# Performance work log

Hardware: AMD Instinct MI355X
Metric: run time of the kernel (lower is better)

## Reference

```python
import jax, jax.numpy as jnp
import numpy as np

HIDDEN = 32
FEATURES = 16
LABELS = 4
T = 8
N = 40000
E = 640000
D_IN = FEATURES + LABELS + HIDDEN + 1  # GATv2Conv input dim = 53


def setup_inputs() -> dict:
    key = jax.random.key(0)
    ks = jax.random.split(key, 16)
    x = jax.random.normal(ks[0], (T, N, FEATURES), dtype=jnp.float32)
    mask = (jax.random.uniform(ks[1], (N,)) < 0.7).astype(jnp.float32)
    labels = jax.random.normal(ks[2], (N, LABELS), dtype=jnp.float32)
    edge_index = jax.random.randint(ks[3], (2, E), 0, N, dtype=jnp.int32)
    edge_weight = jax.random.uniform(ks[4], (E,), dtype=jnp.float32)
    s = 1.0 / np.sqrt(D_IN)
    # 4 GATv2Conv layers stacked: 0=reset, 1=update, 2=cell, 3=final
    Wl = jax.random.normal(ks[5], (4, HIDDEN, D_IN), dtype=jnp.float32) * s
    bl = jnp.zeros((4, HIDDEN), dtype=jnp.float32)
    Wr = jax.random.normal(ks[6], (4, HIDDEN, D_IN), dtype=jnp.float32) * s
    br = jnp.zeros((4, HIDDEN), dtype=jnp.float32)
    att = jax.random.normal(ks[7], (4, HIDDEN), dtype=jnp.float32) * (1.0 / np.sqrt(HIDDEN))
    bconv = jnp.zeros((4, HIDDEN), dtype=jnp.float32)
    W1 = jax.random.normal(ks[8], (FEATURES, HIDDEN), dtype=jnp.float32) * (1.0 / np.sqrt(HIDDEN))
    b1 = jnp.zeros((FEATURES,), dtype=jnp.float32)
    W2 = jax.random.normal(ks[9], (FEATURES, 2 * HIDDEN), dtype=jnp.float32) * (1.0 / np.sqrt(2 * HIDDEN))
    b2 = jnp.zeros((FEATURES,), dtype=jnp.float32)
    return {"x": x, "mask": mask, "labels": labels, "edge_index": edge_index,
            "edge_weight": edge_weight, "Wl": Wl, "bl": bl, "Wr": Wr, "br": br,
            "att": att, "bconv": bconv, "W1": W1, "b1": b1, "W2": W2, "b2": b2}


def gatv2(xin, src, dst, Wl, bl, Wr, br, att, bconv):
    # GATv2Conv, heads=1, add_self_loops=False (edge_weight unused: lin_edge is None)
    xl = xin @ Wl.T + bl          # [N, H] source transform (message)
    xr = xin @ Wr.T + br          # [N, H] target transform
    z = jax.nn.leaky_relu(xl[src] + xr[dst], 0.2)  # [E, H]
    e = z @ att                   # [E] attention logits
    m = jax.ops.segment_max(e, dst, num_segments=N)
    a = jnp.exp(e - m[dst])
    den = jax.ops.segment_sum(a, dst, num_segments=N)[dst]
    a = a / jnp.where(den > 0, den, 1.0)
    out = jax.ops.segment_sum(a[:, None] * xl[src], dst, num_segments=N)
    return out + bconv


def reference(x, mask, labels, edge_index, edge_weight, Wl, bl, Wr, br, att, bconv, W1, b1, W2, b2):
    src, dst = edge_index[0], edge_index[1]
    mcol = mask[:, None]                       # [N, 1] float, concatenated as a feature
    mbool = mcol > 0.5                         # [N, 1] bool, used for where()
    masked_input = jnp.where(mbool[None], x, 0.0)  # [T, N, F]
    hidden0 = jnp.ones((N, HIDDEN), dtype=x.dtype)
    x2_0 = masked_input[0]

    def step(carry, xt):
        hidden, x2 = carry
        ft = jnp.concatenate([x2, mcol, labels], axis=1)        # [N, F+1+L]
        inp = jnp.concatenate([ft, hidden], axis=1)             # [N, D_IN]
        reset = jax.nn.sigmoid(gatv2(inp, src, dst, Wl[0], bl[0], Wr[0], br[0], att[0], bconv[0]))
        update = jax.nn.sigmoid(gatv2(inp, src, dst, Wl[1], bl[1], Wr[1], br[1], att[1], bconv[1]))
        cin = jnp.concatenate([ft, reset * hidden], axis=1)
        cell = jnp.tanh(gatv2(cin, src, dst, Wl[2], bl[2], Wr[2], br[2], att[2], bconv[2]))
        hidden = update * hidden + (1.0 - update) * cell        # (dropout inactive: eval mode)
        y1 = hidden @ W1.T + b1
        x1 = jnp.where(mbool, xt, y1)
        ft2 = jnp.concatenate([x1, mcol, hidden, labels], axis=1)  # [N, D_IN]
        s = jax.nn.relu(gatv2(ft2, src, dst, Wl[3], bl[3], Wr[3], br[3], att[3], bconv[3]))
        y2 = jnp.concatenate([s, hidden], axis=1) @ W2.T + b2
        x2_new = jnp.where(mbool, xt, y2)
        return (hidden, x2_new), x2_new

    _, out = jax.lax.scan(step, (hidden0, x2_0), masked_input)
    return out  # [T, N, F]
```

## Files before the change

### kernel.cpp

```cpp
#include <hip/hip_runtime.h>
#include <math.h>

#define NN   40000
#define EE   640000
#define HID  32
#define FEAT 16
#define LAB  4
#define TT   8
#define DIN  53


__global__ __launch_bounds__(256) void zero_i32(int* __restrict__ p, int n) {
    int i = blockIdx.x * 256 + threadIdx.x;
    if (i < n) p[i] = 0;
}

__global__ __launch_bounds__(256) void hist_kernel(const int* __restrict__ dst,
                                                   int* __restrict__ deg) {
    int e = blockIdx.x * 256 + threadIdx.x;
    if (e < EE) atomicAdd(&deg[dst[e]], 1);
}

__global__ __launch_bounds__(1024) void scan_kernel(const int* __restrict__ deg,
                                                    int* __restrict__ row_ptr) {
    __shared__ int wsum[16];
    __shared__ int chunk_total;
    int tid = threadIdx.x;
    int lane = tid & 63, wv = tid >> 6;
    int carry = 0;
    if (tid == 0) row_ptr[0] = 0;
    for (int base = 0; base < NN; base += 1024) {
        int i = base + tid;
        int v = (i < NN) ? deg[i] : 0;
        #pragma unroll
        for (int o = 1; o < 64; o <<= 1) {
            int t = __shfl_up(v, o);
            if (lane >= o) v += t;
        }
        if (lane == 63) wsum[wv] = v;
        __syncthreads();
        if (tid < 16) {
            int s = wsum[tid];
            #pragma unroll
            for (int o = 1; o < 16; o <<= 1) {
                int t = __shfl_up(s, o);
                if (tid >= o) s += t;
            }
            wsum[tid] = s;
            if (tid == 15) chunk_total = s;
        }
        __syncthreads();
        int woff = (wv == 0) ? 0 : wsum[wv - 1];
        if (i < NN) row_ptr[i + 1] = carry + woff + v;
        carry += chunk_total;
        __syncthreads();
    }
}

__global__ __launch_bounds__(256) void scatter_kernel(const int* __restrict__ src,
                                                      const int* __restrict__ dst,
                                                      const int* __restrict__ row_ptr,
                                                      int* __restrict__ cursor,
                                                      int* __restrict__ csr_src) {
    int e = blockIdx.x * 256 + threadIdx.x;
    if (e < EE) {
        int d = dst[e];
        int pos = atomicAdd(&cursor[d], 1);
        csr_src[row_ptr[d] + pos] = src[e];
    }
}


__global__ __launch_bounds__(256) void init_kernel(const float* __restrict__ x0,
                                                   const float* __restrict__ mask,
                                                   float* __restrict__ hidden,
                                                   float* __restrict__ x2) {
    int i = blockIdx.x * 256 + threadIdx.x;
    if (i < NN * HID) hidden[i] = 1.0f;
    if (i < NN * FEAT) {
        int node = i >> 4;
        x2[i] = (mask[node] > 0.5f) ? x0[i] : 0.0f;
    }
}


template <bool HMUL>
__global__ __launch_bounds__(256) void dense_kernel(const float* __restrict__ feat,
                                                    const float* __restrict__ mask,
                                                    const float* __restrict__ labels,
                                                    const float* __restrict__ hsrc,
                                                    const float* __restrict__ hmul,
                                                    const float* __restrict__ Wl,
                                                    const float* __restrict__ bl,
                                                    const float* __restrict__ Wr,
                                                    const float* __restrict__ br,
                                                    float* __restrict__ xl,
                                                    float* __restrict__ xr) {
    __shared__ float Wl_s[HID * DIN];
    __shared__ float Wr_s[HID * DIN];
    __shared__ float inp_s[8][DIN];
    for (int idx = threadIdx.x; idx < HID * DIN; idx += 256) {
        Wl_s[idx] = Wl[idx];
        Wr_s[idx] = Wr[idx];
    }
    int ni = threadIdx.x >> 5, k = threadIdx.x & 31;
    int node = blockIdx.x * 8 + ni;
    for (int i = k; i < DIN; i += 32) {
        float v;
        if (i < 16)       v = feat[node * 16 + i];
        else if (i == 16) v = mask[node];
        else if (i < 21)  v = labels[node * 4 + (i - 17)];
        else {
            v = hsrc[node * 32 + (i - 21)];
            if (HMUL) v *= hmul[node * 32 + (i - 21)];
        }
        inp_s[ni][i] = v;
    }
    __syncthreads();
    float al = bl[k], ar = br[k];
    const float* wlr = &Wl_s[k * DIN];
    const float* wrr = &Wr_s[k * DIN];
#pragma unroll
    for (int i = 0; i < DIN; ++i) {
        float xv = inp_s[ni][i];
        al += xv * wlr[i];
        ar += xv * wrr[i];
    }
    xl[node * 32 + k] = al;
    xr[node * 32 + k] = ar;
}

template <int ACT>
__global__ __launch_bounds__(256) void conv_kernel(const int* __restrict__ row_ptr,
                                                   const int* __restrict__ csr_src,
                                                   const float* __restrict__ xl,
                                                   const float* __restrict__ xr,
                                                   const float* __restrict__ att,
                                                   const float* __restrict__ bconv,
                                                   float* __restrict__ out) {
    int wid  = threadIdx.x >> 6;
    int lane = threadIdx.x & 63;
    int g = lane >> 2;
    int j = lane & 3;
    int n = blockIdx.x * 4 + wid;
    int c0 = j * 8;
    int beg = row_ptr[n], end = row_ptr[n + 1];

    float4 at0 = *(const float4*)(att + c0);
    float4 at1 = *(const float4*)(att + c0 + 4);
    float4 xr0 = *(const float4*)(xr + n * 32 + c0);
    float4 xr1 = *(const float4*)(xr + n * 32 + c0 + 4);

    float m = -INFINITY, den = 0.0f;
    float acc[8] = {0, 0, 0, 0, 0, 0, 0, 0};

    for (int p = beg + g; p < end; p += 16) {
        int s = csr_src[p];
        const float4* rp = (const float4*)(xl + s * 32 + c0);
        float4 v0 = rp[0];
        float4 v1 = rp[1];
        float part, z;
        z = v0.x + xr0.x; z = (z > 0.f) ? z : 0.2f * z; part  = z * at0.x;
        z = v0.y + xr0.y; z = (z > 0.f) ? z : 0.2f * z; part += z * at0.y;
        z = v0.z + xr0.z; z = (z > 0.f) ? z : 0.2f * z; part += z * at0.z;
        z = v0.w + xr0.w; z = (z > 0.f) ? z : 0.2f * z; part += z * at0.w;
        z = v1.x + xr1.x; z = (z > 0.f) ? z : 0.2f * z; part += z * at1.x;
        z = v1.y + xr1.y; z = (z > 0.f) ? z : 0.2f * z; part += z * at1.y;
        z = v1.z + xr1.z; z = (z > 0.f) ? z : 0.2f * z; part += z * at1.z;
        z = v1.w + xr1.w; z = (z > 0.f) ? z : 0.2f * z; part += z * at1.w;
        part += __shfl_xor(part, 1);
        part += __shfl_xor(part, 2);
        float e = part;
        if (e > m) {
            float sc = __expf(m - e);
            den *= sc;
#pragma unroll
            for (int i = 0; i < 8; ++i) acc[i] *= sc;
            m = e;
        }
        float a = __expf(e - m);
        den += a;
        acc[0] += a * v0.x; acc[1] += a * v0.y; acc[2] += a * v0.z; acc[3] += a * v0.w;
        acc[4] += a * v1.x; acc[5] += a * v1.y; acc[6] += a * v1.z; acc[7] += a * v1.w;
    }

    float o[8];
    if (beg < end) {
        float mt = m;
        mt = fmaxf(mt, __shfl_xor(mt, 4));
        mt = fmaxf(mt, __shfl_xor(mt, 8));
        mt = fmaxf(mt, __shfl_xor(mt, 16));
        mt = fmaxf(mt, __shfl_xor(mt, 32));
        float sc = __expf(m - mt);
        float d = den * sc;
        d += __shfl_xor(d, 4);
        d += __shfl_xor(d, 8);
        d += __shfl_xor(d, 16);
        d += __shfl_xor(d, 32);
#pragma unroll
        for (int i = 0; i < 8; ++i) {
            float t = acc[i] * sc;
            t += __shfl_xor(t, 4);
            t += __shfl_xor(t, 8);
            t += __shfl_xor(t, 16);
            t += __shfl_xor(t, 32);
            o[i] = t / d;
        }
    } else {
#pragma unroll
        for (int i = 0; i < 8; ++i) o[i] = 0.0f;
    }

    if (g == 0) {
        float4 bc0 = *(const float4*)(bconv + c0);
        float4 bc1 = *(const float4*)(bconv + c0 + 4);
        float r[8];
        r[0] = o[0] + bc0.x; r[1] = o[1] + bc0.y; r[2] = o[2] + bc0.z; r[3] = o[3] + bc0.w;
        r[4] = o[4] + bc1.x; r[5] = o[5] + bc1.y; r[6] = o[6] + bc1.z; r[7] = o[7] + bc1.w;
#pragma unroll
        for (int i = 0; i < 8; ++i) {
            if (ACT == 0)      r[i] = 1.0f / (1.0f + __expf(-r[i]));
            else if (ACT == 1) r[i] = tanhf(r[i]);
            else               r[i] = fmaxf(r[i], 0.0f);
        }
        float4* op = (float4*)(out + n * 32 + c0);
        op[0] = make_float4(r[0], r[1], r[2], r[3]);
        op[1] = make_float4(r[4], r[5], r[6], r[7]);
    }
}


__global__ __launch_bounds__(256) void update_dense3_kernel(
        const float* __restrict__ g_update, const float* __restrict__ g_cell,
        float* __restrict__ hidden,
        const float* __restrict__ x_t, const float* __restrict__ mask,
        const float* __restrict__ labels,
        const float* __restrict__ W1, const float* __restrict__ b1,
        const float* __restrict__ Wl3, const float* __restrict__ bl3,
        const float* __restrict__ Wr3, const float* __restrict__ br3,
        float* __restrict__ xl, float* __restrict__ xr) {
    __shared__ float Wl_s[HID * DIN];
    __shared__ float Wr_s[HID * DIN];
    __shared__ float W1_s[FEAT * HID];
    __shared__ float inp_s[8][DIN];
    __shared__ float hs[8][HID + 1];
    for (int idx = threadIdx.x; idx < HID * DIN; idx += 256) {
        Wl_s[idx] = Wl3[idx];
        Wr_s[idx] = Wr3[idx];
    }
    for (int idx = threadIdx.x; idx < FEAT * HID; idx += 256) W1_s[idx] = W1[idx];
    int ni = threadIdx.x >> 5, k = threadIdx.x & 31;
    int node = blockIdx.x * 8 + ni;
    float u = g_update[node * 32 + k];
    float c = g_cell[node * 32 + k];
    float h = hidden[node * 32 + k];
    float hn = u * h + (1.0f - u) * c;
    hidden[node * 32 + k] = hn;
    hs[ni][k] = hn;
    inp_s[ni][17 + k] = hn;
    if (k == 0) inp_s[ni][16] = mask[node];
    if (k < 4)  inp_s[ni][49 + k] = labels[node * 4 + k];
    __syncthreads();
    if (k < 16) {
        float a = b1[k];
        const float* w = &W1_s[k * 32];
#pragma unroll
        for (int i = 0; i < 32; ++i) a += hs[ni][i] * w[i];
        float mv = mask[node];
        inp_s[ni][k] = (mv > 0.5f) ? x_t[node * 16 + k] : a;
    }
    __syncthreads();
    float al = bl3[k], ar = br3[k];
    const float* wl = &Wl_s[k * DIN];
    const float* wr = &Wr_s[k * DIN];
#pragma unroll
    for (int i = 0; i < DIN; ++i) {
        float xv = inp_s[ni][i];
        al += xv * wl[i];
        ar += xv * wr[i];
    }
    xl[node * 32 + k] = al;
    xr[node * 32 + k] = ar;
}


__global__ __launch_bounds__(256) void out_kernel(const float* __restrict__ s,
                                                  const float* __restrict__ hidden,
                                                  const float* __restrict__ W2,
                                                  const float* __restrict__ b2,
                                                  const float* __restrict__ x_t,
                                                  const float* __restrict__ mask,
                                                  float* __restrict__ x2,
                                                  float* __restrict__ out_t) {
    int ni = threadIdx.x >> 4, f = threadIdx.x & 15;
    int node = blockIdx.x * 16 + ni;
    float acc = b2[f];
    const float* srow = s + node * 32;
    const float* hrow = hidden + node * 32;
    const float* w = W2 + f * 64;
#pragma unroll
    for (int i = 0; i < 32; ++i) acc += srow[i] * w[i];
#pragma unroll
    for (int i = 0; i < 32; ++i) acc += hrow[i] * w[32 + i];
    float mv = mask[node];
    float xv = x_t[node * 16 + f];
    float r = (mv > 0.5f) ? xv : acc;
    x2[node * 16 + f] = r;
    out_t[node * 16 + f] = r;
}


extern "C" void kernel_launch(void* const* d_in, const int* in_sizes, int n_in,
                              void* d_out, int out_size, void* d_ws, size_t ws_size,
                              hipStream_t stream) {
    const float* x      = (const float*)d_in[0];
    const float* mask   = (const float*)d_in[1];
    const float* labels = (const float*)d_in[2];
    const int*   src    = (const int*)d_in[3];
    const int*   dst    = src + EE;
    const float* Wl    = (const float*)d_in[5];
    const float* bl    = (const float*)d_in[6];
    const float* Wr    = (const float*)d_in[7];
    const float* br    = (const float*)d_in[8];
    const float* att   = (const float*)d_in[9];
    const float* bconv = (const float*)d_in[10];
    const float* W1    = (const float*)d_in[11];
    const float* b1    = (const float*)d_in[12];
    const float* W2    = (const float*)d_in[13];
    const float* b2    = (const float*)d_in[14];
    float* out = (float*)d_out;

    char* ws = (char*)d_ws;
    size_t off = 0;
    auto alloc = [&](size_t bytes) -> void* {
        void* p = ws + off;
        off = (off + bytes + 255) & ~(size_t)255;
        return p;
    };
    int*   row_ptr = (int*)alloc((NN + 1) * sizeof(int));
    int*   deg     = (int*)alloc(NN * sizeof(int));
    int*   csr_src = (int*)alloc(EE * sizeof(int));
    float* hidden  = (float*)alloc(NN * HID * sizeof(float));
    float* x2      = (float*)alloc(NN * FEAT * sizeof(float));
    float* xl      = (float*)alloc(NN * HID * sizeof(float));
    float* xr      = (float*)alloc(NN * HID * sizeof(float));
    float* g0      = (float*)alloc(NN * HID * sizeof(float));
    float* g1      = (float*)alloc(NN * HID * sizeof(float));
    float* g2      = (float*)alloc(NN * HID * sizeof(float));

    const int WD = HID * DIN;

    zero_i32<<<(NN + 255) / 256, 256, 0, stream>>>(deg, NN);
    hist_kernel<<<EE / 256, 256, 0, stream>>>(dst, deg);
    scan_kernel<<<1, 1024, 0, stream>>>(deg, row_ptr);
    zero_i32<<<(NN + 255) / 256, 256, 0, stream>>>(deg, NN);
    scatter_kernel<<<EE / 256, 256, 0, stream>>>(src, dst, row_ptr, deg, csr_src);
    init_kernel<<<NN * HID / 256, 256, 0, stream>>>(x, mask, hidden, x2);

    for (int t = 0; t < TT; ++t) {
        const float* xt = x + (size_t)t * NN * FEAT;
        float* out_t = out + (size_t)t * NN * FEAT;
        dense_kernel<false><<<NN / 8, 256, 0, stream>>>(x2, mask, labels, hidden, nullptr,
            Wl + 0 * WD, bl + 0 * HID, Wr + 0 * WD, br + 0 * HID, xl, xr);
        conv_kernel<0><<<NN / 4, 256, 0, stream>>>(row_ptr, csr_src, xl, xr,
            att + 0 * HID, bconv + 0 * HID, g0);
        dense_kernel<false><<<NN / 8, 256, 0, stream>>>(x2, mask, labels, hidden, nullptr,
            Wl + 1 * WD, bl + 1 * HID, Wr + 1 * WD, br + 1 * HID, xl, xr);
        conv_kernel<0><<<NN / 4, 256, 0, stream>>>(row_ptr, csr_src, xl, xr,
            att + 1 * HID, bconv + 1 * HID, g1);
        dense_kernel<true><<<NN / 8, 256, 0, stream>>>(x2, mask, labels, hidden, g0,
            Wl + 2 * WD, bl + 2 * HID, Wr + 2 * WD, br + 2 * HID, xl, xr);
        conv_kernel<1><<<NN / 4, 256, 0, stream>>>(row_ptr, csr_src, xl, xr,
            att + 2 * HID, bconv + 2 * HID, g2);
        update_dense3_kernel<<<NN / 8, 256, 0, stream>>>(g1, g2, hidden, xt, mask, labels,
            W1, b1, Wl + 3 * WD, bl + 3 * HID, Wr + 3 * WD, br + 3 * HID, xl, xr);
        conv_kernel<2><<<NN / 4, 256, 0, stream>>>(row_ptr, csr_src, xl, xr,
            att + 3 * HID, bconv + 3 * HID, g0);
        out_kernel<<<NN / 16, 256, 0, stream>>>(g0, hidden, W2, b2, xt, mask, x2, out_t);
    }
}
```

Baseline: 1.999 ms.

## Fuse reset/update GATv2 layers and fold output projection into final conv

The reset and update gates share the same input, so their dense transforms and edge-aggregation passes are merged into one kernel each. The two layers' features are stored interleaved as 64-wide rows, so a single CSR traversal gathers both. The final conv kernel now also computes the W2 output projection and mask select in-register via shuffles, which removes out_kernel and the round trip of the s buffer through memory. The trade-offs are more registers and LDS per block in the merged kernels, possibly lower occupancy, and a W2 transpose load on every conv3 block.

```diff
diff --git a/kernel.cpp b/kernel.cpp
--- a/kernel.cpp
+++ b/kernel.cpp
@@ -8,6 +8,7 @@
 #define LAB  4
 #define TT   8
 #define DIN  53
+#define WD   (HID * DIN)
 
 
 __global__ __launch_bounds__(256) void zero_i32(int* __restrict__ p, int n) {
@@ -84,7 +85,55 @@
 }
 
 
-template <bool HMUL>
+__global__ __launch_bounds__(256) void dense01_kernel(const float* __restrict__ feat,
+                                                      const float* __restrict__ mask,
+                                                      const float* __restrict__ labels,
+                                                      const float* __restrict__ hsrc,
+                                                      const float* __restrict__ Wl,
+                                                      const float* __restrict__ bl,
+                                                      const float* __restrict__ Wr,
+                                                      const float* __restrict__ br,
+                                                      float* __restrict__ xl01,
+                                                      float* __restrict__ xr01) {
+    __shared__ float W_s[4 * WD];
+    __shared__ float inp_s[8][DIN];
+    for (int idx = threadIdx.x; idx < WD; idx += 256) {
+        W_s[idx]          = Wl[idx];
+        W_s[WD + idx]     = Wl[WD + idx];
+        W_s[2 * WD + idx] = Wr[idx];
+        W_s[3 * WD + idx] = Wr[WD + idx];
+    }
+    int ni = threadIdx.x >> 5, k = threadIdx.x & 31;
+    int node = blockIdx.x * 8 + ni;
+    for (int i = k; i < DIN; i += 32) {
+        float v;
+        if (i < 16)       v = feat[node * 16 + i];
+        else if (i == 16) v = mask[node];
+        else if (i < 21)  v = labels[node * 4 + (i - 17)];
+        else              v = hsrc[node * 32 + (i - 21)];
+        inp_s[ni][i] = v;
+    }
+    __syncthreads();
+    float l0 = bl[k], l1 = bl[HID + k], r0 = br[k], r1 = br[HID + k];
+    const float* w0 = &W_s[k * DIN];
+    const float* w1 = &W_s[WD + k * DIN];
+    const float* w2 = &W_s[2 * WD + k * DIN];
+    const float* w3 = &W_s[3 * WD + k * DIN];
+#pragma unroll
+    for (int i = 0; i < DIN; ++i) {
+        float xv = inp_s[ni][i];
+        l0 += xv * w0[i];
+        l1 += xv * w1[i];
+        r0 += xv * w2[i];
+        r1 += xv * w3[i];
+    }
+    xl01[node * 64 + k]      = l0;
+    xl01[node * 64 + 32 + k] = l1;
+    xr01[node * 64 + k]      = r0;
+    xr01[node * 64 + 32 + k] = r1;
+}
+
+
 __global__ __launch_bounds__(256) void dense_kernel(const float* __restrict__ feat,
                                                     const float* __restrict__ mask,
                                                     const float* __restrict__ labels,
@@ -96,10 +145,10 @@
                                                     const float* __restrict__ br,
                                                     float* __restrict__ xl,
                                                     float* __restrict__ xr) {
-    __shared__ float Wl_s[HID * DIN];
-    __shared__ float Wr_s[HID * DIN];
+    __shared__ float Wl_s[WD];
+    __shared__ float Wr_s[WD];
     __shared__ float inp_s[8][DIN];
-    for (int idx = threadIdx.x; idx < HID * DIN; idx += 256) {
+    for (int idx = threadIdx.x; idx < WD; idx += 256) {
         Wl_s[idx] = Wl[idx];
         Wr_s[idx] = Wr[idx];
     }
@@ -110,10 +159,7 @@
         if (i < 16)       v = feat[node * 16 + i];
         else if (i == 16) v = mask[node];
         else if (i < 21)  v = labels[node * 4 + (i - 17)];
-        else {
-            v = hsrc[node * 32 + (i - 21)];
-            if (HMUL) v *= hmul[node * 32 + (i - 21)];
-        }
+        else              v = hsrc[node * 32 + (i - 21)] * hmul[node * 32 + (i - 21)];
         inp_s[ni][i] = v;
     }
     __syncthreads();
@@ -130,62 +176,42 @@
     xr[node * 32 + k] = ar;
 }
 
-template <int ACT>
-__global__ __launch_bounds__(256) void conv_kernel(const int* __restrict__ row_ptr,
-                                                   const int* __restrict__ csr_src,
-                                                   const float* __restrict__ xl,
-                                                   const float* __restrict__ xr,
-                                                   const float* __restrict__ att,
-                                                   const float* __restrict__ bconv,
-                                                   float* __restrict__ out) {
-    int wid  = threadIdx.x >> 6;
-    int lane = threadIdx.x & 63;
-    int g = lane >> 2;
-    int j = lane & 3;
-    int n = blockIdx.x * 4 + wid;
-    int c0 = j * 8;
-    int beg = row_ptr[n], end = row_ptr[n + 1];
-
-    float4 at0 = *(const float4*)(att + c0);
-    float4 at1 = *(const float4*)(att + c0 + 4);
-    float4 xr0 = *(const float4*)(xr + n * 32 + c0);
-    float4 xr1 = *(const float4*)(xr + n * 32 + c0 + 4);
-
-    float m = -INFINITY, den = 0.0f;
-    float acc[8] = {0, 0, 0, 0, 0, 0, 0, 0};
-
-    for (int p = beg + g; p < end; p += 16) {
-        int s = csr_src[p];
-        const float4* rp = (const float4*)(xl + s * 32 + c0);
-        float4 v0 = rp[0];
-        float4 v1 = rp[1];
-        float part, z;
-        z = v0.x + xr0.x; z = (z > 0.f) ? z : 0.2f * z; part  = z * at0.x;
-        z = v0.y + xr0.y; z = (z > 0.f) ? z : 0.2f * z; part += z * at0.y;
-        z = v0.z + xr0.z; z = (z > 0.f) ? z : 0.2f * z; part += z * at0.z;
-        z = v0.w + xr0.w; z = (z > 0.f) ? z : 0.2f * z; part += z * at0.w;
-        z = v1.x + xr1.x; z = (z > 0.f) ? z : 0.2f * z; part += z * at1.x;
-        z = v1.y + xr1.y; z = (z > 0.f) ? z : 0.2f * z; part += z * at1.y;
-        z = v1.z + xr1.z; z = (z > 0.f) ? z : 0.2f * z; part += z * at1.z;
-        z = v1.w + xr1.w; z = (z > 0.f) ? z : 0.2f * z; part += z * at1.w;
-        part += __shfl_xor(part, 1);
-        part += __shfl_xor(part, 2);
-        float e = part;
-        if (e > m) {
-            float sc = __expf(m - e);
-            den *= sc;
-#pragma unroll
-            for (int i = 0; i < 8; ++i) acc[i] *= sc;
-            m = e;
-        }
-        float a = __expf(e - m);
-        den += a;
-        acc[0] += a * v0.x; acc[1] += a * v0.y; acc[2] += a * v0.z; acc[3] += a * v0.w;
-        acc[4] += a * v1.x; acc[5] += a * v1.y; acc[6] += a * v1.z; acc[7] += a * v1.w;
-    }
-
-    float o[8];
-    if (beg < end) {
+
+__device__ __forceinline__ float edge_score(const float4& v0, const float4& v1,
+                                            const float4& xr0, const float4& xr1,
+                                            const float4& at0, const float4& at1) {
+    float part, z;
+    z = v0.x + xr0.x; z = (z > 0.f) ? z : 0.2f * z; part  = z * at0.x;
+    z = v0.y + xr0.y; z = (z > 0.f) ? z : 0.2f * z; part += z * at0.y;
+    z = v0.z + xr0.z; z = (z > 0.f) ? z : 0.2f * z; part += z * at0.z;
+    z = v0.w + xr0.w; z = (z > 0.f) ? z : 0.2f * z; part += z * at0.w;
+    z = v1.x + xr1.x; z = (z > 0.f) ? z : 0.2f * z; part += z * at1.x;
+    z = v1.y + xr1.y; z = (z > 0.f) ? z : 0.2f * z; part += z * at1.y;
+    z = v1.z + xr1.z; z = (z > 0.f) ? z : 0.2f * z; part += z * at1.z;
+    z = v1.w + xr1.w; z = (z > 0.f) ? z : 0.2f * z; part += z * at1.w;
+    part += __shfl_xor(part, 1);
+    part += __shfl_xor(part, 2);
+    return part;
+}
+
+__device__ __forceinline__ void online_update(float e, float& m, float& den, float* acc,
+                                              const float4& v0, const float4& v1) {
+    if (e > m) {
+        float sc = __expf(m - e);
+        den *= sc;
+#pragma unroll
+        for (int i = 0; i < 8; ++i) acc[i] *= sc;
+        m = e;
+    }
+    float a = __expf(e - m);
+    den += a;
+    acc[0] += a * v0.x; acc[1] += a * v0.y; acc[2] += a * v0.z; acc[3] += a * v0.w;
+    acc[4] += a * v1.x; acc[5] += a * v1.y; acc[6] += a * v1.z; acc[7] += a * v1.w;
+}
+
+__device__ __forceinline__ void merge_groups(float m, float den, const float* acc,
+                                             bool nonempty, float* o) {
+    if (nonempty) {
         float mt = m;
         mt = fmaxf(mt, __shfl_xor(mt, 4));
         mt = fmaxf(mt, __shfl_xor(mt, 8));
@@ -210,22 +236,194 @@
 #pragma unroll
         for (int i = 0; i < 8; ++i) o[i] = 0.0f;
     }
+}
+
+
+__global__ __launch_bounds__(256) void conv01_kernel(const int* __restrict__ row_ptr,
+                                                     const int* __restrict__ csr_src,
+                                                     const float* __restrict__ xl01,
+                                                     const float* __restrict__ xr01,
+                                                     const float* __restrict__ att,
+                                                     const float* __restrict__ bconv,
+                                                     float* __restrict__ g0,
+                                                     float* __restrict__ g1) {
+    int wid  = threadIdx.x >> 6;
+    int lane = threadIdx.x & 63;
+    int g = lane >> 2, j = lane & 3;
+    int n = blockIdx.x * 4 + wid;
+    int c0 = j * 8;
+    int beg = row_ptr[n], end = row_ptr[n + 1];
+
+    float4 a00 = *(const float4*)(att + c0);
+    float4 a01 = *(const float4*)(att + c0 + 4);
+    float4 a10 = *(const float4*)(att + 32 + c0);
+    float4 a11 = *(const float4*)(att + 32 + c0 + 4);
+    const float* xrn = xr01 + n * 64;
+    float4 xr00 = *(const float4*)(xrn + c0);
+    float4 xr01v = *(const float4*)(xrn + c0 + 4);
+    float4 xr10 = *(const float4*)(xrn + 32 + c0);
+    float4 xr11 = *(const float4*)(xrn + 32 + c0 + 4);
+
+    float m0 = -INFINITY, den0 = 0.0f, acc0[8] = {0, 0, 0, 0, 0, 0, 0, 0};
+    float m1 = -INFINITY, den1 = 0.0f, acc1[8] = {0, 0, 0, 0, 0, 0, 0, 0};
+
+    for (int p = beg + g; p < end; p += 16) {
+        int s = csr_src[p];
+        const float4* rp = (const float4*)(xl01 + s * 64 + c0);
+        const float4* rq = (const float4*)(xl01 + s * 64 + 32 + c0);
+        float4 v00 = rp[0], v01 = rp[1];
+        float4 v10 = rq[0], v11 = rq[1];
+        float e0 = edge_score(v00, v01, xr00, xr01v, a00, a01);
+        float e1 = edge_score(v10, v11, xr10, xr11, a10, a11);
+        online_update(e0, m0, den0, acc0, v00, v01);
+        online_update(e1, m1, den1, acc1, v10, v11);
+    }
+
+    float o0[8], o1[8];
+    bool ne = beg < end;
+    merge_groups(m0, den0, acc0, ne, o0);
+    merge_groups(m1, den1, acc1, ne, o1);
+
+    if (g == 0) {
+        float4 b00 = *(const float4*)(bconv + c0);
+        float4 b01 = *(const float4*)(bconv + c0 + 4);
+        float4 b10 = *(const float4*)(bconv + 32 + c0);
+        float4 b11 = *(const float4*)(bconv + 32 + c0 + 4);
+        float r0[8] = {o0[0] + b00.x, o0[1] + b00.y, o0[2] + b00.z, o0[3] + b00.w,
+                       o0[4] + b01.x, o0[5] + b01.y, o0[6] + b01.z, o0[7] + b01.w};
+        float r1[8] = {o1[0] + b10.x, o1[1] + b10.y, o1[2] + b10.z, o1[3] + b10.w,
+                       o1[4] + b11.x, o1[5] + b11.y, o1[6] + b11.z, o1[7] + b11.w};
+#pragma unroll
+        for (int i = 0; i < 8; ++i) {
+            r0[i] = 1.0f / (1.0f + __expf(-r0[i]));
+            r1[i] = 1.0f / (1.0f + __expf(-r1[i]));
+        }
+        float4* p0 = (float4*)(g0 + n * 32 + c0);
+        p0[0] = make_float4(r0[0], r0[1], r0[2], r0[3]);
+        p0[1] = make_float4(r0[4], r0[5], r0[6], r0[7]);
+        float4* p1 = (float4*)(g1 + n * 32 + c0);
+        p1[0] = make_float4(r1[0], r1[1], r1[2], r1[3]);
+        p1[1] = make_float4(r1[4], r1[5], r1[6], r1[7]);
+    }
+}
+
+
+__global__ __launch_bounds__(256) void conv2_kernel(const int* __restrict__ row_ptr,
+                                                    const int* __restrict__ csr_src,
+                                                    const float* __restrict__ xl,
+                                                    const float* __restrict__ xr,
+                                                    const float* __restrict__ att,
+                                                    const float* __restrict__ bconv,
+                                                    float* __restrict__ out) {
+    int wid  = threadIdx.x >> 6;
+    int lane = threadIdx.x & 63;
+    int g = lane >> 2, j = lane & 3;
+    int n = blockIdx.x * 4 + wid;
+    int c0 = j * 8;
+    int beg = row_ptr[n], end = row_ptr[n + 1];
+
+    float4 at0 = *(const float4*)(att + c0);
+    float4 at1 = *(const float4*)(att + c0 + 4);
+    float4 xr0 = *(const float4*)(xr + n * 32 + c0);
+    float4 xr1 = *(const float4*)(xr + n * 32 + c0 + 4);
+
+    float m = -INFINITY, den = 0.0f, acc[8] = {0, 0, 0, 0, 0, 0, 0, 0};
+    for (int p = beg + g; p < end; p += 16) {
+        int s = csr_src[p];
+        const float4* rp = (const float4*)(xl + s * 32 + c0);
+        float4 v0 = rp[0], v1 = rp[1];
+        float e = edge_score(v0, v1, xr0, xr1, at0, at1);
+        online_update(e, m, den, acc, v0, v1);
+    }
+    float o[8];
+    merge_groups(m, den, acc, beg < end, o);
 
     if (g == 0) {
         float4 bc0 = *(const float4*)(bconv + c0);
         float4 bc1 = *(const float4*)(bconv + c0 + 4);
-        float r[8];
-        r[0] = o[0] + bc0.x; r[1] = o[1] + bc0.y; r[2] = o[2] + bc0.z; r[3] = o[3] + bc0.w;
-        r[4] = o[4] + bc1.x; r[5] = o[5] + bc1.y; r[6] = o[6] + bc1.z; r[7] = o[7] + bc1.w;
-#pragma unroll
-        for (int i = 0; i < 8; ++i) {
-            if (ACT == 0)      r[i] = 1.0f / (1.0f + __expf(-r[i]));
-            else if (ACT == 1) r[i] = tanhf(r[i]);
-            else               r[i] = fmaxf(r[i], 0.0f);
-        }
+        float r[8] = {o[0] + bc0.x, o[1] + bc0.y, o[2] + bc0.z, o[3] + bc0.w,
+                      o[4] + bc1.x, o[5] + bc1.y, o[6] + bc1.z, o[7] + bc1.w};
+#pragma unroll
+        for (int i = 0; i < 8; ++i) r[i] = tanhf(r[i]);
         float4* op = (float4*)(out + n * 32 + c0);
         op[0] = make_float4(r[0], r[1], r[2], r[3]);
         op[1] = make_float4(r[4], r[5], r[6], r[7]);
+    }
+}
+
+
+__global__ __launch_bounds__(256) void conv3_out_kernel(const int* __restrict__ row_ptr,
+                                                        const int* __restrict__ csr_src,
+                                                        const float* __restrict__ xl,
+                                                        const float* __restrict__ xr,
+                                                        const float* __restrict__ att,
+                                                        const float* __restrict__ bconv,
+                                                        const float* __restrict__ hidden,
+                                                        const float* __restrict__ W2,
+                                                        const float* __restrict__ b2,
+                                                        const float* __restrict__ x_t,
+                                                        const float* __restrict__ mask,
+                                                        float* __restrict__ x2,
+                                                        float* __restrict__ out_t) {
+    __shared__ float W2s[64 * 16];
+    for (int idx = threadIdx.x; idx < 64 * 16; idx += 256) {
+        int f = idx & 15, c = idx >> 4;
+        W2s[c * 16 + f] = W2[f * 64 + c];
+    }
+    __syncthreads();
+
+    int wid  = threadIdx.x >> 6;
+    int lane = threadIdx.x & 63;
+    int g = lane >> 2, j = lane & 3;
+    int n = blockIdx.x * 4 + wid;
+    int c0 = j * 8;
+    int beg = row_ptr[n], end = row_ptr[n + 1];
+
+    float4 at0 = *(const float4*)(att + c0);
+    float4 at1 = *(const float4*)(att + c0 + 4);
+    float4 xr0 = *(const float4*)(xr + n * 32 + c0);
+    float4 xr1 = *(const float4*)(xr + n * 32 + c0 + 4);
+
+    float m = -INFINITY, den = 0.0f, acc[8] = {0, 0, 0, 0, 0, 0, 0, 0};
+    for (int p = beg + g; p < end; p += 16) {
+        int s = csr_src[p];
+        const float4* rp = (const float4*)(xl + s * 32 + c0);
+        float4 v0 = rp[0], v1 = rp[1];
+        float e = edge_score(v0, v1, xr0, xr1, at0, at1);
+        online_update(e, m, den, acc, v0, v1);
+    }
+    float o[8];
+    merge_groups(m, den, acc, beg < end, o);
+
+    float4 bc0 = *(const float4*)(bconv + c0);
+    float4 bc1 = *(const float4*)(bconv + c0 + 4);
+    float r[8] = {fmaxf(o[0] + bc0.x, 0.f), fmaxf(o[1] + bc0.y, 0.f),
+                  fmaxf(o[2] + bc0.z, 0.f), fmaxf(o[3] + bc0.w, 0.f),
+                  fmaxf(o[4] + bc1.x, 0.f), fmaxf(o[5] + bc1.y, 0.f),
+                  fmaxf(o[6] + bc1.z, 0.f), fmaxf(o[7] + bc1.w, 0.f)};
+    float4 h0 = *(const float4*)(hidden + n * 32 + c0);
+    float4 h1 = *(const float4*)(hidden + n * 32 + c0 + 4);
+    float hv[8] = {h0.x, h0.y, h0.z, h0.w, h1.x, h1.y, h1.z, h1.w};
+
+    int f = lane & 15;
+    int base = lane & ~3;
+    float y = b2[f];
+#pragma unroll
+    for (int j2 = 0; j2 < 4; ++j2) {
+#pragma unroll
+        for (int i = 0; i < 8; ++i) {
+            float sv = __shfl(r[i], base + j2);
+            float hh = __shfl(hv[i], base + j2);
+            int c = j2 * 8 + i;
+            y += sv * W2s[c * 16 + f] + hh * W2s[(32 + c) * 16 + f];
+        }
+    }
+    if (lane < 16) {
+        float mv = mask[n];
+        float xv = x_t[n * 16 + f];
+        float rr = (mv > 0.5f) ? xv : y;
+        x2[n * 16 + f] = rr;
+        out_t[n * 16 + f] = rr;
     }
 }
 
@@ -239,12 +437,12 @@
         const float* __restrict__ Wl3, const float* __restrict__ bl3,
         const float* __restrict__ Wr3, const float* __restrict__ br3,
         float* __restrict__ xl, float* __restrict__ xr) {
-    __shared__ float Wl_s[HID * DIN];
-    __shared__ float Wr_s[HID * DIN];
+    __shared__ float Wl_s[WD];
+    __shared__ float Wr_s[WD];
     __shared__ float W1_s[FEAT * HID];
     __shared__ float inp_s[8][DIN];
     __shared__ float hs[8][HID + 1];
-    for (int idx = threadIdx.x; idx < HID * DIN; idx += 256) {
+    for (int idx = threadIdx.x; idx < WD; idx += 256) {
         Wl_s[idx] = Wl3[idx];
         Wr_s[idx] = Wr3[idx];
     }
@@ -281,32 +479,6 @@
     }
     xl[node * 32 + k] = al;
     xr[node * 32 + k] = ar;
-}
-
-
-__global__ __launch_bounds__(256) void out_kernel(const float* __restrict__ s,
-                                                  const float* __restrict__ hidden,
-                                                  const float* __restrict__ W2,
-                                                  const float* __restrict__ b2,
-                                                  const float* __restrict__ x_t,
-                                                  const float* __restrict__ mask,
-                                                  float* __restrict__ x2,
-                                                  float* __restrict__ out_t) {
-    int ni = threadIdx.x >> 4, f = threadIdx.x & 15;
-    int node = blockIdx.x * 16 + ni;
-    float acc = b2[f];
-    const float* srow = s + node * 32;
-    const float* hrow = hidden + node * 32;
-    const float* w = W2 + f * 64;
-#pragma unroll
-    for (int i = 0; i < 32; ++i) acc += srow[i] * w[i];
-#pragma unroll
-    for (int i = 0; i < 32; ++i) acc += hrow[i] * w[32 + i];
-    float mv = mask[node];
-    float xv = x_t[node * 16 + f];
-    float r = (mv > 0.5f) ? xv : acc;
-    x2[node * 16 + f] = r;
-    out_t[node * 16 + f] = r;
 }
 
 
@@ -342,13 +514,13 @@
     int*   csr_src = (int*)alloc(EE * sizeof(int));
     float* hidden  = (float*)alloc(NN * HID * sizeof(float));
     float* x2      = (float*)alloc(NN * FEAT * sizeof(float));
+    float* xl01    = (float*)alloc(NN * 64 * sizeof(float));
+    float* xr01    = (float*)alloc(NN * 64 * sizeof(float));
     float* xl      = (float*)alloc(NN * HID * sizeof(float));
     float* xr      = (float*)alloc(NN * HID * sizeof(float));
     float* g0      = (float*)alloc(NN * HID * sizeof(float));
     float* g1      = (float*)alloc(NN * HID * sizeof(float));
     float* g2      = (float*)alloc(NN * HID * sizeof(float));
-
-    const int WD = HID * DIN;
 
     zero_i32<<<(NN + 255) / 256, 256, 0, stream>>>(deg, NN);
     hist_kernel<<<EE / 256, 256, 0, stream>>>(dst, deg);
@@ -360,22 +532,17 @@
     for (int t = 0; t < TT; ++t) {
         const float* xt = x + (size_t)t * NN * FEAT;
         float* out_t = out + (size_t)t * NN * FEAT;
-        dense_kernel<false><<<NN / 8, 256, 0, stream>>>(x2, mask, labels, hidden, nullptr,
-            Wl + 0 * WD, bl + 0 * HID, Wr + 0 * WD, br + 0 * HID, xl, xr);
-        conv_kernel<0><<<NN / 4, 256, 0, stream>>>(row_ptr, csr_src, xl, xr,
-            att + 0 * HID, bconv + 0 * HID, g0);
-        dense_kernel<false><<<NN / 8, 256, 0, stream>>>(x2, mask, labels, hidden, nullptr,
-            Wl + 1 * WD, bl + 1 * HID, Wr + 1 * WD, br + 1 * HID, xl, xr);
-        conv_kernel<0><<<NN / 4, 256, 0, stream>>>(row_ptr, csr_src, xl, xr,
-            att + 1 * HID, bconv + 1 * HID, g1);
-        dense_kernel<true><<<NN / 8, 256, 0, stream>>>(x2, mask, labels, hidden, g0,
+        dense01_kernel<<<NN / 8, 256, 0, stream>>>(x2, mask, labels, hidden,
+            Wl, bl, Wr, br, xl01, xr01);
+        conv01_kernel<<<NN / 4, 256, 0, stream>>>(row_ptr, csr_src, xl01, xr01,
+            att, bconv, g0, g1);
+        dense_kernel<<<NN / 8, 256, 0, stream>>>(x2, mask, labels, hidden, g0,
             Wl + 2 * WD, bl + 2 * HID, Wr + 2 * WD, br + 2 * HID, xl, xr);
-        conv_kernel<1><<<NN / 4, 256, 0, stream>>>(row_ptr, csr_src, xl, xr,
+        conv2_kernel<<<NN / 4, 256, 0, stream>>>(row_ptr, csr_src, xl, xr,
             att + 2 * HID, bconv + 2 * HID, g2);
         update_dense3_kernel<<<NN / 8, 256, 0, stream>>>(g1, g2, hidden, xt, mask, labels,
             W1, b1, Wl + 3 * WD, bl + 3 * HID, Wr + 3 * WD, br + 3 * HID, xl, xr);
-        conv_kernel<2><<<NN / 4, 256, 0, stream>>>(row_ptr, csr_src, xl, xr,
-            att + 3 * HID, bconv + 3 * HID, g0);
-        out_kernel<<<NN / 16, 256, 0, stream>>>(g0, hidden, W2, b2, xt, mask, x2, out_t);
-    }
-}
+        conv3_out_kernel<<<NN / 4, 256, 0, stream>>>(row_ptr, csr_src, xl, xr,
+            att + 3 * HID, bconv + 3 * HID, hidden, W2, b2, xt, mask, x2, out_t);
+    }
+}
```

Result: slower. 2.052 ms (+2.7%).
